# Kernel tuning notes

Hardware: AMD Instinct MI355X
Metric: run time of the kernel (lower is better)

Reference implementation:

```python
import jax, jax.numpy as jnp
import numpy as np
from jax import lax

B, C, H, W = 32, 256, 56, 56
EPS = 1e-5


def ste_sign(x):
    # Binarize with clipped straight-through estimator (ReActNet style):
    # forward = sign(x), backward = 1 where |x| < 1.
    c = jnp.clip(x, -1.0, 1.0)
    return c + lax.stop_gradient(jnp.sign(x) - c)


def rsign(x, beta):
    # per-channel learnable shift then binarize; beta: [C]
    return ste_sign(x - beta[None, :, None, None])


def scaled_sign_weight(w):
    # w: [Cout, Cin, k, k] -> alpha * sign(w), alpha = mean|w| per filter
    alpha = jnp.mean(jnp.abs(w), axis=(1, 2, 3), keepdims=True)
    sw = w + lax.stop_gradient(jnp.sign(w) - w)  # STE through sign
    return alpha * sw


def conv2d(x, w, padding):
    return lax.conv_general_dilated(
        x, w, window_strides=(1, 1), padding=[(padding, padding)] * 2,
        dimension_numbers=("NCHW", "OIHW", "NCHW"))


def bn(x, g, b, m, v):
    inv = g / jnp.sqrt(v + EPS)
    return x * inv[None, :, None, None] + (b - m * inv)[None, :, None, None]


def rprelu(x, gamma, slope, zeta):
    # RPReLU: PReLU(x - gamma) + zeta, all per-channel
    y = x - gamma[None, :, None, None]
    return jnp.where(y > 0, y, slope[None, :, None, None] * y) + zeta[None, :, None, None]


def setup_inputs() -> dict:
    key = jax.random.key(0)
    ks = jax.random.split(key, 12)
    return {
        "x": jax.random.normal(ks[0], (B, C, H, W), jnp.float32),
        "rsign1_beta": jax.random.normal(ks[1], (C,), jnp.float32) * 0.1,
        "w1": jax.random.normal(ks[2], (C, C, 3, 3), jnp.float32) * 0.05,
        "bn1_g": jnp.ones((C,), jnp.float32),
        "bn1_b": jnp.zeros((C,), jnp.float32),
        "bn1_m": jax.random.normal(ks[3], (C,), jnp.float32) * 0.1,
        "bn1_v": jax.random.uniform(ks[4], (C,), jnp.float32) + 0.5,
        "rsign2_beta": jax.random.normal(ks[5], (C,), jnp.float32) * 0.1,
        "w2": jax.random.normal(ks[6], (C, C, 1, 1), jnp.float32) * 0.05,
        "bn2_g": jnp.ones((C,), jnp.float32),
        "bn2_b": jnp.zeros((C,), jnp.float32),
        "bn2_m": jax.random.normal(ks[7], (C,), jnp.float32) * 0.1,
        "bn2_v": jax.random.uniform(ks[8], (C,), jnp.float32) + 0.5,
        "pr_gamma": jax.random.normal(ks[9], (C,), jnp.float32) * 0.1,
        "pr_slope": jnp.full((C,), 0.25, jnp.float32),
        "pr_zeta": jax.random.normal(ks[10], (C,), jnp.float32) * 0.1,
    }


def reference(x, rsign1_beta, w1, bn1_g, bn1_b, bn1_m, bn1_v,
              rsign2_beta, w2, bn2_g, bn2_b, bn2_m, bn2_v,
              pr_gamma, pr_slope, pr_zeta):
    # layer1: RSign -> binarized 3x3 conv -> BN, + residual, RPReLU
    out = bn(conv2d(rsign(x, rsign1_beta), scaled_sign_weight(w1), 1),
             bn1_g, bn1_b, bn1_m, bn1_v)
    out = out + x
    out_r = rprelu(out, pr_gamma, pr_slope, pr_zeta)
    # layer2: RSign -> binarized 1x1 conv -> BN, + residual, RPReLU (shared params)
    out = bn(conv2d(rsign(out_r, rsign2_beta), scaled_sign_weight(w2), 0),
             bn2_g, bn2_b, bn2_m, bn2_v)
    out = out + out_r
    return rprelu(out, pr_gamma, pr_slope, pr_zeta)
```

## Files before the change

### kernel.cpp

```cpp
#include <hip/hip_runtime.h>
#include <stdint.h>

#define BB 32
#define CC_ 256
#define HH 56
#define WW 56
#define EPSV 1e-5f

typedef unsigned long long u64;

__global__ __launch_bounds__(256) void prep_weights(
    const float* __restrict__ w1, const float* __restrict__ w2,
    const float* __restrict__ bn1_g, const float* __restrict__ bn1_b,
    const float* __restrict__ bn1_m, const float* __restrict__ bn1_v,
    const float* __restrict__ bn2_g, const float* __restrict__ bn2_b,
    const float* __restrict__ bn2_m, const float* __restrict__ bn2_v,
    u64* __restrict__ pw1, u64* __restrict__ pw2,
    float* __restrict__ scale1, float* __restrict__ shift1,
    float* __restrict__ scale2, float* __restrict__ shift2)
{
    int co = blockIdx.x;
    int ci = threadIdx.x;
    int wv = ci >> 6, lane = ci & 63;

    float wvals[9];
    const float* wp = w1 + ((size_t)co*256 + ci)*9;
    float s1 = 0.f;
#pragma unroll
    for (int t = 0; t < 9; ++t) { wvals[t] = wp[t]; s1 += fabsf(wvals[t]); }
    float v2 = w2[(size_t)co*256 + ci];
    float s2 = fabsf(v2);

#pragma unroll
    for (int t = 0; t < 9; ++t) {
        u64 b = __ballot(wvals[t] > 0.0f);
        if (lane == 0) pw1[((size_t)co*9 + t)*4 + wv] = b;
    }
    {
        u64 b = __ballot(v2 > 0.0f);
        if (lane == 0) pw2[(size_t)co*4 + wv] = b;
    }

    for (int off = 32; off > 0; off >>= 1) {
        s1 += __shfl_down(s1, off);
        s2 += __shfl_down(s2, off);
    }
    __shared__ float r1[4], r2[4];
    if (lane == 0) { r1[wv] = s1; r2[wv] = s2; }
    __syncthreads();
    if (ci == 0) {
        float a1 = (r1[0]+r1[1]+r1[2]+r1[3]) * (1.0f/2304.0f);
        float a2 = (r2[0]+r2[1]+r2[2]+r2[3]) * (1.0f/256.0f);
        float inv1 = bn1_g[co] / sqrtf(bn1_v[co] + EPSV);
        float inv2 = bn2_g[co] / sqrtf(bn2_v[co] + EPSV);
        scale1[co] = a1 * inv1;
        shift1[co] = bn1_b[co] - bn1_m[co]*inv1;
        scale2[co] = a2 * inv2;
        shift2[co] = bn2_b[co] - bn2_m[co]*inv2;
    }
}

__global__ __launch_bounds__(256) void pack_input(
    const float* __restrict__ x, const float* __restrict__ beta1,
    u64* __restrict__ pack1)
{
    int bid = blockIdx.x;
    int n = bid / HH, h = bid % HH;
    int wv = threadIdx.x >> 6, lane = threadIdx.x & 63;
    int c = wv*64 + lane;
    const float4* row = (const float4*)(x + (((size_t)n*CC_ + c)*HH + h)*WW);
    float beta = beta1[c];
    u64 mine = 0;
#pragma unroll
    for (int g = 0; g < 14; ++g) {
        float4 v = row[g];
        u64 b0 = __ballot(v.x > beta);
        u64 b1 = __ballot(v.y > beta);
        u64 b2 = __ballot(v.z > beta);
        u64 b3 = __ballot(v.w > beta);
        int w0 = g*4;
        if (lane == w0)   mine = b0;
        if (lane == w0+1) mine = b1;
        if (lane == w0+2) mine = b2;
        if (lane == w0+3) mine = b3;
    }
    if (lane < WW) pack1[((size_t)bid*WW + lane)*4 + wv] = mine;
}

__global__ __launch_bounds__(256, 2) void main_fused(
    const float* __restrict__ x,
    const u64* __restrict__ pack1,
    const u64* __restrict__ pw1, const u64* __restrict__ pw2,
    const float* __restrict__ scale1, const float* __restrict__ shift1,
    const float* __restrict__ scale2, const float* __restrict__ shift2,
    const float* __restrict__ beta2,
    const float* __restrict__ pr_gamma, const float* __restrict__ pr_slope,
    const float* __restrict__ pr_zeta,
    float* __restrict__ out)
{
    __shared__ u64 rows[3][WW][4];
    __shared__ float outr[CC_][WW+1];
    __shared__ u64 p2[WW][4];

    int bid = blockIdx.x;
    int n = bid / HH, h = bid % HH;
    int tid = threadIdx.x;
    int wv = tid >> 6;
    int lane = tid & 63;
    int cc = tid;

    u64 wr1[36];
    {
        const u64* wq1 = pw1 + (size_t)cc*36;
#pragma unroll
        for (int j = 0; j < 18; ++j) {
            ulonglong2 v = *(const ulonglong2*)(wq1 + 2*j);
            wr1[2*j] = v.x; wr1[2*j+1] = v.y;
        }
    }
    u64 wr2[4];
    {
        ulonglong2 a = *(const ulonglong2*)(pw2 + (size_t)cc*4);
        ulonglong2 b = *(const ulonglong2*)(pw2 + (size_t)cc*4 + 2);
        wr2[0]=a.x; wr2[1]=a.y; wr2[2]=b.x; wr2[3]=b.y;
    }
    float sc1 = scale1[cc], sh1 = shift1[cc];
    float sc2 = scale2[cc], sh2 = shift2[cc];
    float gam = pr_gamma[cc], slp = pr_slope[cc], zet = pr_zeta[cc];
    float bet2 = beta2[cc];

    {
        int hm = (h > 0) ? h-1 : 0;
        int hp = (h < HH-1) ? h+1 : HH-1;
        for (int idx = tid; idx < 3*WW*4; idx += 256) {
            int r = idx / (WW*4);
            int rem = idx - r*(WW*4);
            int hr = (r == 0) ? hm : ((r == 1) ? h : hp);
            ((u64*)rows)[idx] = pack1[((size_t)(n*HH + hr)*WW)*4 + rem];
        }
    }
    for (int idx = tid; idx < CC_*14; idx += 256) {
        int c = idx / 14, g = idx - c*14;
        float4 v = *(const float4*)(x + (((size_t)n*CC_ + c)*HH + h)*WW + 4*g);
        outr[c][4*g+0] = v.x; outr[c][4*g+1] = v.y;
        outr[c][4*g+2] = v.z; outr[c][4*g+3] = v.w;
    }
    __syncthreads();

    bool rowU = (h > 0), rowD = (h < HH-1);
    for (int w = 0; w < WW; ++w) {
        bool colL = (w > 0), colR = (w < WW-1);
        int wm = colL ? w-1 : w;
        int wp = colR ? w+1 : w;
        bool tv[9];
        tv[0] = rowU && colL; tv[1] = rowU; tv[2] = rowU && colR;
        tv[3] = colL;         tv[4] = true; tv[5] = colR;
        tv[6] = rowD && colL; tv[7] = rowD; tv[8] = rowD && colR;

        int acc = 0;
#pragma unroll
        for (int t = 0; t < 9; ++t) {
            int r = t / 3, ci = t - 3*r;
            int wc = (ci == 0) ? wm : ((ci == 1) ? w : wp);
            ulonglong2 a = *(const ulonglong2*)&rows[r][wc][0];
            ulonglong2 b = *(const ulonglong2*)&rows[r][wc][2];
            int p = __builtin_popcountll(a.x ^ wr1[t*4+0])
                  + __builtin_popcountll(a.y ^ wr1[t*4+1])
                  + __builtin_popcountll(b.x ^ wr1[t*4+2])
                  + __builtin_popcountll(b.y ^ wr1[t*4+3]);
            acc += tv[t] ? p : 128;
        }
        float s = (float)(2304 - 2*acc);
        float r0 = outr[cc][w];
        float y = fmaf(s, sc1, sh1) + r0;
        float yr = y - gam;
        float o = (yr > 0.f ? yr : slp*yr) + zet;
        outr[cc][w] = o;
    }

    {
        u64 mine = 0;
        for (int ww = 0; ww < WW; ++ww) {
            u64 b = __ballot(outr[cc][ww] > bet2);
            if (ww == lane) mine = b;
        }
        if (lane < WW) p2[lane][wv] = mine;
    }
    __syncthreads();

    for (int w = 0; w < WW; ++w) {
        ulonglong2 a = *(const ulonglong2*)&p2[w][0];
        ulonglong2 b = *(const ulonglong2*)&p2[w][2];
        int p = __builtin_popcountll(a.x ^ wr2[0]) + __builtin_popcountll(a.y ^ wr2[1])
              + __builtin_popcountll(b.x ^ wr2[2]) + __builtin_popcountll(b.y ^ wr2[3]);
        float s = (float)(256 - 2*p);
        float rr = outr[cc][w];
        float y = fmaf(s, sc2, sh2) + rr;
        float yr = y - gam;
        float o = (yr > 0.f ? yr : slp*yr) + zet;
        outr[cc][w] = o;
    }
    __syncthreads();

    for (int idx = tid; idx < CC_*14; idx += 256) {
        int c = idx / 14, g = idx - c*14;
        float4 v;
        v.x = outr[c][4*g+0]; v.y = outr[c][4*g+1];
        v.z = outr[c][4*g+2]; v.w = outr[c][4*g+3];
        *(float4*)(out + (((size_t)n*CC_ + c)*HH + h)*WW + 4*g) = v;
    }
}

extern "C" void kernel_launch(void* const* d_in, const int* in_sizes, int n_in,
                              void* d_out, int out_size, void* d_ws, size_t ws_size,
                              hipStream_t stream) {
    const float* x           = (const float*)d_in[0];
    const float* rsign1_beta = (const float*)d_in[1];
    const float* w1          = (const float*)d_in[2];
    const float* bn1_g       = (const float*)d_in[3];
    const float* bn1_b       = (const float*)d_in[4];
    const float* bn1_m       = (const float*)d_in[5];
    const float* bn1_v       = (const float*)d_in[6];
    const float* rsign2_beta = (const float*)d_in[7];
    const float* w2          = (const float*)d_in[8];
    const float* bn2_g       = (const float*)d_in[9];
    const float* bn2_b       = (const float*)d_in[10];
    const float* bn2_m       = (const float*)d_in[11];
    const float* bn2_v       = (const float*)d_in[12];
    const float* pr_gamma    = (const float*)d_in[13];
    const float* pr_slope    = (const float*)d_in[14];
    const float* pr_zeta     = (const float*)d_in[15];

    char* ws = (char*)d_ws;
    u64*   pw1    = (u64*)(ws);
    u64*   pw2    = (u64*)(ws + 73728);
    float* scale1 = (float*)(ws + 81920);
    float* shift1 = (float*)(ws + 82944);
    float* scale2 = (float*)(ws + 83968);
    float* shift2 = (float*)(ws + 84992);
    u64*   pack1  = (u64*)(ws + 86016);

    prep_weights<<<256, 256, 0, stream>>>(w1, w2, bn1_g, bn1_b, bn1_m, bn1_v,
                                          bn2_g, bn2_b, bn2_m, bn2_v,
                                          pw1, pw2, scale1, shift1, scale2, shift2);
    pack_input<<<BB*HH, 256, 0, stream>>>(x, rsign1_beta, pack1);
    main_fused<<<BB*HH, 256, 0, stream>>>(x, pack1, pw1, pw2,
                                          scale1, shift1, scale2, shift2,
                                          rsign2_beta, pr_gamma, pr_slope, pr_zeta,
                                          (float*)d_out);
}
```

Before: 387.3 us.

## Split main kernel into half-row tiles, specialize interior rows, stage pack input via LDS

The fused main kernel now handles half an image row (28 columns) per block, with a one-column halo of packed bits. This doubles the grid and cuts shared memory so four blocks per CU can be resident. Interior rows use a branch-free 9-tap popcount loop, with edge columns peeled out, and RPReLU now uses fmin/fmax plus fma. The input-packing kernel first stages the row through LDS for coalesced float4 loads, then ballots per column; the trade-off is more redundant weight register loads across twice as many blocks.

```diff
diff --git a/kernel.cpp b/kernel.cpp
--- a/kernel.cpp
+++ b/kernel.cpp
@@ -5,6 +5,8 @@
 #define CC_ 256
 #define HH 56
 #define WW 56
+#define TW 28
+#define TCOLS 30
 #define EPSV 1e-5f
 
 typedef unsigned long long u64;
@@ -64,30 +66,37 @@
     const float* __restrict__ x, const float* __restrict__ beta1,
     u64* __restrict__ pack1)
 {
+    __shared__ float xrow[CC_][WW+1];
     int bid = blockIdx.x;
     int n = bid / HH, h = bid % HH;
-    int wv = threadIdx.x >> 6, lane = threadIdx.x & 63;
-    int c = wv*64 + lane;
-    const float4* row = (const float4*)(x + (((size_t)n*CC_ + c)*HH + h)*WW);
-    float beta = beta1[c];
+    int tid = threadIdx.x;
+
+    for (int idx = tid; idx < CC_*14; idx += 256) {
+        int c = idx / 14, g = idx - c*14;
+        float4 v = *(const float4*)(x + (((size_t)n*CC_ + c)*HH + h)*WW + 4*g);
+        xrow[c][4*g+0] = v.x; xrow[c][4*g+1] = v.y;
+        xrow[c][4*g+2] = v.z; xrow[c][4*g+3] = v.w;
+    }
+    __syncthreads();
+
+    int wv = tid >> 6, lane = tid & 63;
+    float beta = beta1[wv*64 + lane];
     u64 mine = 0;
-#pragma unroll
-    for (int g = 0; g < 14; ++g) {
-        float4 v = row[g];
-        u64 b0 = __ballot(v.x > beta);
-        u64 b1 = __ballot(v.y > beta);
-        u64 b2 = __ballot(v.z > beta);
-        u64 b3 = __ballot(v.w > beta);
-        int w0 = g*4;
-        if (lane == w0)   mine = b0;
-        if (lane == w0+1) mine = b1;
-        if (lane == w0+2) mine = b2;
-        if (lane == w0+3) mine = b3;
+    for (int ww = 0; ww < WW; ++ww) {
+        u64 b = __ballot(xrow[wv*64 + lane][ww] > beta);
+        if (ww == lane) mine = b;
     }
     if (lane < WW) pack1[((size_t)bid*WW + lane)*4 + wv] = mine;
 }
 
-__global__ __launch_bounds__(256, 2) void main_fused(
+__device__ __forceinline__ int tap_pop(const u64* __restrict__ col, const u64* __restrict__ wr) {
+    ulonglong2 a = *(const ulonglong2*)(col);
+    ulonglong2 b = *(const ulonglong2*)(col + 2);
+    return __builtin_popcountll(a.x ^ wr[0]) + __builtin_popcountll(a.y ^ wr[1])
+         + __builtin_popcountll(b.x ^ wr[2]) + __builtin_popcountll(b.y ^ wr[3]);
+}
+
+__global__ __launch_bounds__(256, 4) void main_fused(
     const float* __restrict__ x,
     const u64* __restrict__ pack1,
     const u64* __restrict__ pw1, const u64* __restrict__ pw2,
@@ -98,12 +107,15 @@
     const float* __restrict__ pr_zeta,
     float* __restrict__ out)
 {
-    __shared__ u64 rows[3][WW][4];
-    __shared__ float outr[CC_][WW+1];
-    __shared__ u64 p2[WW][4];
+    __shared__ u64 rows[3][TCOLS][4];
+    __shared__ float outr[CC_][TW+1];
+    __shared__ u64 p2[TW][4];
 
     int bid = blockIdx.x;
-    int n = bid / HH, h = bid % HH;
+    int tile = bid & 1;
+    int nh = bid >> 1;
+    int n = nh / HH, h = nh % HH;
+    int w0 = tile * TW;
     int tid = threadIdx.x;
     int wv = tid >> 6;
     int lane = tid & 63;
@@ -132,82 +144,113 @@
     {
         int hm = (h > 0) ? h-1 : 0;
         int hp = (h < HH-1) ? h+1 : HH-1;
-        for (int idx = tid; idx < 3*WW*4; idx += 256) {
-            int r = idx / (WW*4);
-            int rem = idx - r*(WW*4);
+        for (int idx = tid; idx < 3*TCOLS*4; idx += 256) {
+            int r = idx / (TCOLS*4);
+            int rem = idx - r*(TCOLS*4);
+            int j = rem >> 2, q = rem & 3;
+            int gw = w0 - 1 + j;
+            gw = (gw < 0) ? 0 : ((gw > WW-1) ? WW-1 : gw);
             int hr = (r == 0) ? hm : ((r == 1) ? h : hp);
-            ((u64*)rows)[idx] = pack1[((size_t)(n*HH + hr)*WW)*4 + rem];
-        }
-    }
-    for (int idx = tid; idx < CC_*14; idx += 256) {
-        int c = idx / 14, g = idx - c*14;
-        float4 v = *(const float4*)(x + (((size_t)n*CC_ + c)*HH + h)*WW + 4*g);
+            rows[r][j][q] = pack1[((size_t)(n*HH + hr)*WW + gw)*4 + q];
+        }
+    }
+    for (int idx = tid; idx < CC_*7; idx += 256) {
+        int c = idx / 7, g = idx - c*7;
+        float4 v = *(const float4*)(x + (((size_t)n*CC_ + c)*HH + h)*WW + w0 + 4*g);
         outr[c][4*g+0] = v.x; outr[c][4*g+1] = v.y;
         outr[c][4*g+2] = v.z; outr[c][4*g+3] = v.w;
     }
     __syncthreads();
 
     bool rowU = (h > 0), rowD = (h < HH-1);
-    for (int w = 0; w < WW; ++w) {
-        bool colL = (w > 0), colR = (w < WW-1);
-        int wm = colL ? w-1 : w;
-        int wp = colR ? w+1 : w;
-        bool tv[9];
-        tv[0] = rowU && colL; tv[1] = rowU; tv[2] = rowU && colR;
-        tv[3] = colL;         tv[4] = true; tv[5] = colR;
-        tv[6] = rowD && colL; tv[7] = rowD; tv[8] = rowD && colR;
-
-        int acc = 0;
-#pragma unroll
-        for (int t = 0; t < 9; ++t) {
-            int r = t / 3, ci = t - 3*r;
-            int wc = (ci == 0) ? wm : ((ci == 1) ? w : wp);
-            ulonglong2 a = *(const ulonglong2*)&rows[r][wc][0];
-            ulonglong2 b = *(const ulonglong2*)&rows[r][wc][2];
-            int p = __builtin_popcountll(a.x ^ wr1[t*4+0])
-                  + __builtin_popcountll(a.y ^ wr1[t*4+1])
-                  + __builtin_popcountll(b.x ^ wr1[t*4+2])
-                  + __builtin_popcountll(b.y ^ wr1[t*4+3]);
-            acc += tv[t] ? p : 128;
-        }
-        float s = (float)(2304 - 2*acc);
-        float r0 = outr[cc][w];
-        float y = fmaf(s, sc1, sh1) + r0;
-        float yr = y - gam;
-        float o = (yr > 0.f ? yr : slp*yr) + zet;
-        outr[cc][w] = o;
+
+    if (rowU && rowD) {
+        int pstart = 0, pend = TW;
+        if (tile == 0) {
+            int acc = 0;
+#pragma unroll
+            for (int r = 0; r < 3; ++r) {
+                acc += tap_pop(&rows[r][1][0], &wr1[(r*3+1)*4]);
+                acc += tap_pop(&rows[r][2][0], &wr1[(r*3+2)*4]);
+            }
+            float s = (float)(1536 - 2*acc);
+            float y = fmaf(s, sc1, sh1) + outr[cc][0];
+            float yr = y - gam;
+            outr[cc][0] = fmaf(slp, fminf(yr, 0.f), fmaxf(yr, 0.f)) + zet;
+            pstart = 1;
+        } else {
+            int acc = 0;
+#pragma unroll
+            for (int r = 0; r < 3; ++r) {
+                acc += tap_pop(&rows[r][TW-1][0], &wr1[(r*3+0)*4]);
+                acc += tap_pop(&rows[r][TW][0],   &wr1[(r*3+1)*4]);
+            }
+            float s = (float)(1536 - 2*acc);
+            float y = fmaf(s, sc1, sh1) + outr[cc][TW-1];
+            float yr = y - gam;
+            outr[cc][TW-1] = fmaf(slp, fminf(yr, 0.f), fmaxf(yr, 0.f)) + zet;
+            pend = TW-1;
+        }
+        for (int p = pstart; p < pend; ++p) {
+            int acc = 0;
+#pragma unroll
+            for (int r = 0; r < 3; ++r) {
+#pragma unroll
+                for (int dc = 0; dc < 3; ++dc)
+                    acc += tap_pop(&rows[r][p+dc][0], &wr1[(r*3+dc)*4]);
+            }
+            float s = (float)(2304 - 2*acc);
+            float y = fmaf(s, sc1, sh1) + outr[cc][p];
+            float yr = y - gam;
+            outr[cc][p] = fmaf(slp, fminf(yr, 0.f), fmaxf(yr, 0.f)) + zet;
+        }
+    } else {
+        for (int p = 0; p < TW; ++p) {
+            int w = w0 + p;
+            bool colL = (w > 0), colR = (w < WW-1);
+            int acc = 0, nval = 0;
+#pragma unroll
+            for (int t = 0; t < 9; ++t) {
+                int r = t / 3, dc = t - 3*r;
+                bool v = ((r == 0) ? rowU : (r == 2) ? rowD : true)
+                      && ((dc == 0) ? colL : (dc == 2) ? colR : true);
+                if (v) { acc += tap_pop(&rows[r][p+dc][0], &wr1[t*4]); ++nval; }
+            }
+            float s = (float)(256*nval - 2*acc);
+            float y = fmaf(s, sc1, sh1) + outr[cc][p];
+            float yr = y - gam;
+            outr[cc][p] = fmaf(slp, fminf(yr, 0.f), fmaxf(yr, 0.f)) + zet;
+        }
     }
 
     {
         u64 mine = 0;
-        for (int ww = 0; ww < WW; ++ww) {
+        for (int ww = 0; ww < TW; ++ww) {
             u64 b = __ballot(outr[cc][ww] > bet2);
             if (ww == lane) mine = b;
         }
-        if (lane < WW) p2[lane][wv] = mine;
-    }
-    __syncthreads();
-
-    for (int w = 0; w < WW; ++w) {
-        ulonglong2 a = *(const ulonglong2*)&p2[w][0];
-        ulonglong2 b = *(const ulonglong2*)&p2[w][2];
-        int p = __builtin_popcountll(a.x ^ wr2[0]) + __builtin_popcountll(a.y ^ wr2[1])
-              + __builtin_popcountll(b.x ^ wr2[2]) + __builtin_popcountll(b.y ^ wr2[3]);
-        float s = (float)(256 - 2*p);
-        float rr = outr[cc][w];
-        float y = fmaf(s, sc2, sh2) + rr;
+        if (lane < TW) p2[lane][wv] = mine;
+    }
+    __syncthreads();
+
+    for (int p = 0; p < TW; ++p) {
+        ulonglong2 a = *(const ulonglong2*)&p2[p][0];
+        ulonglong2 b = *(const ulonglong2*)&p2[p][2];
+        int pc = __builtin_popcountll(a.x ^ wr2[0]) + __builtin_popcountll(a.y ^ wr2[1])
+               + __builtin_popcountll(b.x ^ wr2[2]) + __builtin_popcountll(b.y ^ wr2[3]);
+        float s = (float)(256 - 2*pc);
+        float y = fmaf(s, sc2, sh2) + outr[cc][p];
         float yr = y - gam;
-        float o = (yr > 0.f ? yr : slp*yr) + zet;
-        outr[cc][w] = o;
-    }
-    __syncthreads();
-
-    for (int idx = tid; idx < CC_*14; idx += 256) {
-        int c = idx / 14, g = idx - c*14;
+        outr[cc][p] = fmaf(slp, fminf(yr, 0.f), fmaxf(yr, 0.f)) + zet;
+    }
+    __syncthreads();
+
+    for (int idx = tid; idx < CC_*7; idx += 256) {
+        int c = idx / 7, g = idx - c*7;
         float4 v;
         v.x = outr[c][4*g+0]; v.y = outr[c][4*g+1];
         v.z = outr[c][4*g+2]; v.w = outr[c][4*g+3];
-        *(float4*)(out + (((size_t)n*CC_ + c)*HH + h)*WW + 4*g) = v;
+        *(float4*)(out + (((size_t)n*CC_ + c)*HH + h)*WW + w0 + 4*g) = v;
     }
 }
 
@@ -244,8 +287,8 @@
                                           bn2_g, bn2_b, bn2_m, bn2_v,
                                           pw1, pw2, scale1, shift1, scale2, shift2);
     pack_input<<<BB*HH, 256, 0, stream>>>(x, rsign1_beta, pack1);
-    main_fused<<<BB*HH, 256, 0, stream>>>(x, pack1, pw1, pw2,
-                                          scale1, shift1, scale2, shift2,
-                                          rsign2_beta, pr_gamma, pr_slope, pr_zeta,
-                                          (float*)d_out);
-}
+    main_fused<<<BB*HH*2, 256, 0, stream>>>(x, pack1, pw1, pw2,
+                                            scale1, shift1, scale2, shift2,
+                                            rsign2_beta, pr_gamma, pr_slope, pr_zeta,
+                                            (float*)d_out);
+}
```

Result: no change. 381.5 us (-1.5%).
